# Kernel tuning notes

Hardware: AMD Instinct MI355X
Metric: run time of the kernel (lower is better)

## Reference

```python
import jax, jax.numpy as jnp
import numpy as np

N_NODES = 100000
N_EDGES = 1600000
HIDDEN = 128
NUM_FEAT = 1
NUM_CLASSES = 10
NUM_GRAPHS = 512


def setup_inputs() -> dict:
    key = jax.random.key(0)
    ks = jax.random.split(key, 16)
    x = jax.random.normal(ks[0], (N_NODES, NUM_FEAT), dtype=jnp.float32)
    edge_index = jax.random.randint(ks[1], (2, N_EDGES), 0, N_NODES, dtype=jnp.int64)
    batch = jnp.sort(jax.random.randint(ks[2], (N_NODES,), 0, NUM_GRAPHS, dtype=jnp.int64))
    def glorot(k, shape):
        lim = float(np.sqrt(6.0 / (shape[0] + shape[1])))
        return jax.random.uniform(k, shape, jnp.float32, -lim, lim)
    params = {
        'W1': glorot(ks[3], (NUM_FEAT, HIDDEN)), 'b1': jnp.zeros((HIDDEN,), jnp.float32),
        'W2': glorot(ks[4], (HIDDEN, HIDDEN)), 'b2': jnp.zeros((HIDDEN,), jnp.float32),
        'W3': glorot(ks[5], (HIDDEN, HIDDEN)), 'b3': jnp.zeros((HIDDEN,), jnp.float32),
        'W4': glorot(ks[6], (HIDDEN, HIDDEN)), 'b4': jnp.zeros((HIDDEN,), jnp.float32),
        'W5': glorot(ks[7], (HIDDEN, HIDDEN)), 'b5': jnp.zeros((HIDDEN,), jnp.float32),
        'Wlin': glorot(ks[8], (HIDDEN, NUM_CLASSES)), 'blin': jnp.zeros((NUM_CLASSES,), jnp.float32),
    }
    return {'x': x, 'edge_index': edge_index, 'batch': batch, **params}


def _gcn_norm(edge_index, n_nodes):
    # PyG GCNConv: add self-loops, sym-normalize by deg^-1/2 on both ends.
    loops = jnp.arange(n_nodes, dtype=edge_index.dtype)
    src = jnp.concatenate([edge_index[0], loops])
    dst = jnp.concatenate([edge_index[1], loops])
    deg = jax.ops.segment_sum(jnp.ones_like(dst, jnp.float32), dst, num_segments=n_nodes)
    dis = jnp.where(deg > 0, jax.lax.rsqrt(jnp.maximum(deg, 1.0)), 0.0)
    norm = dis[src] * dis[dst]  # [E + N]
    return src, dst, norm


def _gcn_conv(h, W, b, src, dst, norm, n_nodes):
    h = h @ W  # transform first (PyG order)
    msg = h[src] * norm[:, None]  # gather + scale, [E+N, H]
    out = jax.ops.segment_sum(msg, dst, num_segments=n_nodes)  # scatter-add
    return out + b


def reference(x, edge_index, batch, W1, b1, W2, b2, W3, b3, W4, b4, W5, b5, Wlin, blin):
    n = x.shape[0]
    src, dst, norm = _gcn_norm(edge_index, n)
    h = _gcn_conv(x, W1, b1, src, dst, norm, n)
    h = _gcn_conv(h, W2, b2, src, dst, norm, n)
    h = _gcn_conv(h, W3, b3, src, dst, norm, n)
    h = _gcn_conv(h, W4, b4, src, dst, norm, n)
    h = _gcn_conv(h, W5, b5, src, dst, norm, n)
    # global mean pool over graphs
    sums = jax.ops.segment_sum(h, batch, num_segments=NUM_GRAPHS)
    cnts = jax.ops.segment_sum(jnp.ones((n,), jnp.float32), batch, num_segments=NUM_GRAPHS)
    pooled = sums / jnp.maximum(cnts, 1.0)[:, None]
    # dropout is identity at eval
    return pooled @ Wlin + blin
```

## Files before the change

### kernel.cpp

```cpp
#include <hip/hip_runtime.h>

#define NT 256
#define BN_SHIFT 8
#define NBUCKET_MAX 512
#define CAP 8192
#define EPB 4096

__global__ void __launch_bounds__(768)
prep_kernel(const float* __restrict__ W1, const float* __restrict__ b1,
            const float* __restrict__ W2, const float* __restrict__ b2,
            const float* __restrict__ W3, const float* __restrict__ b3,
            const float* __restrict__ W4, const float* __restrict__ b4,
            const float* __restrict__ W5, const float* __restrict__ b5,
            const float* __restrict__ Wlin, float* __restrict__ qout,
            int* __restrict__ gcur, int NB) {
  __shared__ float cur[6][128];
  __shared__ float red[6][10][8];
  const int tid = threadIdx.x;
  for (int i = tid; i < NB; i += 768) gcur[i] = 0;
  const int vi = tid >> 7;
  const int t = tid & 127;
  float init;
  if (vi == 0) init = W1[t];
  else if (vi == 1) init = b1[t];
  else if (vi == 2) init = b2[t];
  else if (vi == 3) init = b3[t];
  else if (vi == 4) init = b4[t];
  else init = b5[t];
  cur[vi][t] = init;
  __syncthreads();
  const float* Ws[4] = {W2, W3, W4, W5};
  #pragma unroll
  for (int l = 0; l < 4; ++l) {
    const int nact = l + 2;
    float s = 0.f;
    if (vi < nact) {
      const float* __restrict__ W = Ws[l];
      #pragma unroll 64
      for (int k = 0; k < 128; ++k) s += cur[vi][k] * W[k * 128 + t];
    }
    __syncthreads();
    if (vi < nact) cur[vi][t] = s;
    __syncthreads();
  }
  if (tid < 480) {
    int v = tid / 80, rem = tid % 80, c = rem >> 3, pp = rem & 7;
    float s = 0.f;
    #pragma unroll
    for (int k = 0; k < 16; ++k) {
      int kk = pp * 16 + k;
      s += cur[v][kk] * Wlin[kk * 10 + c];
    }
    red[v][c][pp] = s;
  }
  __syncthreads();
  if (tid < 60) {
    int v = tid / 10, c = tid % 10;
    float s = 0.f;
    #pragma unroll
    for (int p = 0; p < 8; ++p) s += red[v][c][p];
    qout[v * 10 + c] = s;
  }
}

__global__ void binA_kernel(const int* __restrict__ ei, int* __restrict__ gcur,
                            unsigned int* __restrict__ dump, int E, int NB) {
  __shared__ unsigned int cnt[NBUCKET_MAX];
  __shared__ unsigned int base[NBUCKET_MAX];
  const int t = threadIdx.x;
  const int e0 = blockIdx.x * EPB;
  const bool vec_ok = ((E & 3) == 0);
  for (int b = t; b < NB; b += 256) cnt[b] = 0;
  __syncthreads();
  unsigned int slot[16];
  unsigned int dreg[16];
  #pragma unroll
  for (int jj = 0; jj < 4; ++jj) {
    int e = e0 + jj * 1024 + t * 4;
    if (vec_ok && e + 3 < E) {
      int4 d4 = *reinterpret_cast<const int4*>(&ei[E + e]);
      dreg[jj * 4 + 0] = (unsigned)d4.x;
      dreg[jj * 4 + 1] = (unsigned)d4.y;
      dreg[jj * 4 + 2] = (unsigned)d4.z;
      dreg[jj * 4 + 3] = (unsigned)d4.w;
      #pragma unroll
      for (int k = 0; k < 4; ++k)
        slot[jj * 4 + k] = atomicAdd(&cnt[dreg[jj * 4 + k] >> BN_SHIFT], 1u);
    } else {
      #pragma unroll
      for (int k = 0; k < 4; ++k) {
        int ee = e + k;
        if (ee < E) {
          unsigned d = (unsigned)ei[E + ee];
          dreg[jj * 4 + k] = d;
          slot[jj * 4 + k] = atomicAdd(&cnt[d >> BN_SHIFT], 1u);
        }
      }
    }
  }
  __syncthreads();
  for (int b = t; b < NB; b += 256) {
    unsigned int c = cnt[b];
    base[b] = c ? (unsigned int)atomicAdd(&gcur[b], (int)c) : 0u;
  }
  __syncthreads();
  #pragma unroll
  for (int jj = 0; jj < 4; ++jj) {
    int e = e0 + jj * 1024 + t * 4;
    unsigned s4v[4];
    bool fast = (vec_ok && e + 3 < E);
    if (fast) {
      int4 s4 = *reinterpret_cast<const int4*>(&ei[e]);
      s4v[0] = (unsigned)s4.x; s4v[1] = (unsigned)s4.y;
      s4v[2] = (unsigned)s4.z; s4v[3] = (unsigned)s4.w;
    }
    #pragma unroll
    for (int k = 0; k < 4; ++k) {
      int ee = e + k;
      if (ee < E) {
        unsigned s = fast ? s4v[k] : (unsigned)ei[ee];
        unsigned d = dreg[jj * 4 + k];
        unsigned b = d >> BN_SHIFT;
        unsigned pos = base[b] + slot[jj * 4 + k];
        if (pos < CAP)
          dump[(size_t)b * CAP + pos] = (s << BN_SHIFT) | (d & 255u);
      }
    }
  }
}

__global__ void binB_kernel(const unsigned int* __restrict__ dump,
                            const int* __restrict__ gcur,
                            const float* __restrict__ x, int* __restrict__ col,
                            int2* __restrict__ rl, float* __restrict__ dis2,
                            float* __restrict__ sq, float2* __restrict__ ta, int N) {
  __shared__ int cnt[256];
  __shared__ int sc[256];
  __shared__ int cur[256];
  const int b = blockIdx.x, t = threadIdx.x;
  cnt[t] = 0;
  __syncthreads();
  int total = gcur[b];
  if (total > CAP) total = CAP;
  const unsigned int* seg = dump + (size_t)b * CAP;
  unsigned wreg[CAP / 256];
  #pragma unroll
  for (int k = 0; k < CAP / 256; ++k) {
    int i = (k << 8) + t;
    if (i < total) {
      unsigned w = seg[i];
      wreg[k] = w;
      atomicAdd(&cnt[w & 255u], 1);
    }
  }
  __syncthreads();
  int v = cnt[t];
  sc[t] = v;
  __syncthreads();
  for (int off = 1; off < 256; off <<= 1) {
    int u = (t >= off) ? sc[t - off] : 0;
    __syncthreads();
    sc[t] += u;
    __syncthreads();
  }
  int rbase = b * CAP + sc[t] - v;
  cur[t] = rbase;
  __syncthreads();
  #pragma unroll
  for (int k = 0; k < CAP / 256; ++k) {
    int i = (k << 8) + t;
    if (i < total) {
      unsigned w = wreg[k];
      int slot = atomicAdd(&cur[w & 255u], 1);
      col[slot] = (int)(w >> BN_SHIFT);
    }
  }
  int node = (b << BN_SHIFT) + t;
  if (node < N) {
    rl[node] = make_int2(rbase, v);
    float dis = rsqrtf((float)v + 1.0f);
    dis2[node] = dis * dis;
    sq[node] = 1.0f / dis;
    ta[node] = make_float2(dis * x[node], dis);
  }
}

__global__ void gather_kernel(const int* __restrict__ col, const int2* __restrict__ rl,
                              const float* __restrict__ dis2,
                              const float2* __restrict__ tin, float2* __restrict__ tout,
                              float* __restrict__ ssave, int N) {
  int tid = blockIdx.x * blockDim.x + threadIdx.x;
  int node = tid >> 3, l8 = tid & 7;
  if (node >= N) return;
  int2 r = rl[node];
  float sx = 0.f, sy = 0.f;
  int j = l8;
  for (; j + 8 < r.y; j += 16) {
    int c0 = col[r.x + j];
    int c1 = col[r.x + j + 8];
    float2 a0 = tin[c0];
    float2 a1 = tin[c1];
    sx += a0.x + a1.x;
    sy += a0.y + a1.y;
  }
  if (j < r.y) {
    float2 a = tin[col[r.x + j]];
    sx += a.x;
    sy += a.y;
  }
  sx += __shfl_xor(sx, 1);
  sx += __shfl_xor(sx, 2);
  sx += __shfl_xor(sx, 4);
  sy += __shfl_xor(sy, 1);
  sy += __shfl_xor(sy, 2);
  sy += __shfl_xor(sy, 4);
  if (l8 == 0) {
    float2 ts = tin[node];
    float m = dis2[node];
    float oy = m * (sy + ts.y);
    tout[node] = make_float2(m * (sx + ts.x), oy);
    if (ssave) ssave[node] = oy;
  }
}

__device__ __forceinline__ int lower_bound_i(const int* a, int n, int key) {
  int lo = 0, hi = n;
  while (lo < hi) {
    int mid = (lo + hi) >> 1;
    if (a[mid] < key) lo = mid + 1; else hi = mid;
  }
  return lo;
}

__global__ void pool_kernel(const int* __restrict__ batch, int N,
                            const float2* __restrict__ t5, const float* __restrict__ s4,
                            const float* __restrict__ s3, const float* __restrict__ s2,
                            const float* __restrict__ s1, const float* __restrict__ sq,
                            const float* __restrict__ q, const float* __restrict__ blin,
                            float* __restrict__ out) {
  int g = blockIdx.x;
  __shared__ int sh[2];
  if (threadIdx.x == 0) {
    sh[0] = lower_bound_i(batch, N, g);
    sh[1] = lower_bound_i(batch, N, g + 1);
  }
  __syncthreads();
  int lo = sh[0], hi = sh[1];
  float a[5] = {0.f, 0.f, 0.f, 0.f, 0.f};
  for (int i = lo + threadIdx.x; i < hi; i += blockDim.x) {
    float qq = sq[i];
    a[0] += t5[i].x * qq;
    a[1] += s4[i] * qq;
    a[2] += s3[i] * qq;
    a[3] += s2[i] * qq;
    a[4] += s1[i] * qq;
  }
  __shared__ float red[4][5];
  __shared__ float m5[5];
  int lane = threadIdx.x & 63, wave = threadIdx.x >> 6;
  #pragma unroll
  for (int j = 0; j < 5; ++j)
    #pragma unroll
    for (int o = 32; o > 0; o >>= 1) a[j] += __shfl_down(a[j], o);
  if (lane == 0)
    #pragma unroll
    for (int j = 0; j < 5; ++j) red[wave][j] = a[j];
  __syncthreads();
  if (threadIdx.x == 0) {
    float denom = fmaxf((float)(hi - lo), 1.0f);
    #pragma unroll
    for (int j = 0; j < 5; ++j)
      m5[j] = (red[0][j] + red[1][j] + red[2][j] + red[3][j]) / denom;
  }
  __syncthreads();
  int t = threadIdx.x;
  if (t < 10) {
    out[g * 10 + t] = m5[0] * q[t] + m5[1] * q[10 + t] + m5[2] * q[20 + t] +
                      m5[3] * q[30 + t] + m5[4] * q[40 + t] + q[50 + t] + blin[t];
  }
}

extern "C" void kernel_launch(void* const* d_in, const int* in_sizes, int n_in,
                              void* d_out, int out_size, void* d_ws, size_t ws_size,
                              hipStream_t stream) {
  const float* x    = (const float*)d_in[0];
  const int*   ei   = (const int*)d_in[1];
  const int*   batch= (const int*)d_in[2];
  const float* W1   = (const float*)d_in[3];
  const float* b1   = (const float*)d_in[4];
  const float* W2   = (const float*)d_in[5];
  const float* b2   = (const float*)d_in[6];
  const float* W3   = (const float*)d_in[7];
  const float* b3   = (const float*)d_in[8];
  const float* W4   = (const float*)d_in[9];
  const float* b4   = (const float*)d_in[10];
  const float* W5   = (const float*)d_in[11];
  const float* b5   = (const float*)d_in[12];
  const float* Wlin = (const float*)d_in[13];
  const float* blin = (const float*)d_in[14];

  const int N  = in_sizes[0];
  const int E  = in_sizes[1] / 2;
  const int G  = out_size / 10;
  const int NB = (N + 255) >> BN_SHIFT;

  float* ws = (float*)d_ws;
  size_t off = 0;
  float2* ta   = (float2*)(ws + off); off += 2 * (size_t)N;
  float2* tb   = (float2*)(ws + off); off += 2 * (size_t)N;
  float*  dis2 = ws + off;            off += N;
  float*  sq   = ws + off;            off += N;
  float*  s1   = ws + off;            off += N;
  float*  s2   = ws + off;            off += N;
  float*  s3   = ws + off;            off += N;
  float*  s4   = ws + off;            off += N;
  float*  qv   = ws + off;            off += 64;
  if (off & 1) off++;
  int2* rl     = (int2*)(ws + off);   off += 2 * (size_t)N;
  int* gcur    = (int*)(ws + off);    off += NB;
  if (off & 1) off++;
  unsigned int* dump = (unsigned int*)(ws + off); off += (size_t)NB * CAP;
  int* col     = (int*)(ws + off);    off += (size_t)NB * CAP;
  (void)ws_size;

  const int gridA = (E + EPB - 1) / EPB;
  const int gridG = (8 * N + NT - 1) / NT;

  prep_kernel<<<1, 768, 0, stream>>>(W1, b1, W2, b2, W3, b3, W4, b4, W5, b5,
                                     Wlin, qv, gcur, NB);
  binA_kernel<<<gridA, 256, 0, stream>>>(ei, gcur, dump, E, NB);
  binB_kernel<<<NB, 256, 0, stream>>>(dump, gcur, x, col, rl, dis2, sq, ta, N);

  gather_kernel<<<gridG, NT, 0, stream>>>(col, rl, dis2, ta, tb, s1, N);
  gather_kernel<<<gridG, NT, 0, stream>>>(col, rl, dis2, tb, ta, s2, N);
  gather_kernel<<<gridG, NT, 0, stream>>>(col, rl, dis2, ta, tb, s3, N);
  gather_kernel<<<gridG, NT, 0, stream>>>(col, rl, dis2, tb, ta, s4, N);
  gather_kernel<<<gridG, NT, 0, stream>>>(col, rl, dis2, ta, tb, nullptr, N);

  pool_kernel<<<G, 256, 0, stream>>>(batch, N, tb, s4, s3, s2, s1, sq, qv, blin,
                                     (float*)d_out);
}
```

Before: 116.1 us.

## Replace CSR gather with per-bucket shared-memory atomic scatter over binned edges

binB no longer builds a CSR (col/rl) via counting sort and only computes degrees. The five propagation layers now read the bucketed edge dump directly: each 1024-thread block owns a 256-node bucket and accumulates neighbor values into shared memory with float atomics. The last layer skips the unused y channel. This removes the per-edge col write and the sort pass, but brings LDS atomic contention and non-deterministic float summation order.

After: 165.5 us. +42.5%, slower.

```diff
diff --git a/kernel.cpp b/kernel.cpp
--- a/kernel.cpp
+++ b/kernel.cpp
@@ -131,95 +131,76 @@
 
 __global__ void binB_kernel(const unsigned int* __restrict__ dump,
                             const int* __restrict__ gcur,
-                            const float* __restrict__ x, int* __restrict__ col,
-                            int2* __restrict__ rl, float* __restrict__ dis2,
+                            const float* __restrict__ x, float* __restrict__ dis2,
                             float* __restrict__ sq, float2* __restrict__ ta, int N) {
   __shared__ int cnt[256];
-  __shared__ int sc[256];
-  __shared__ int cur[256];
   const int b = blockIdx.x, t = threadIdx.x;
   cnt[t] = 0;
   __syncthreads();
   int total = gcur[b];
   if (total > CAP) total = CAP;
   const unsigned int* seg = dump + (size_t)b * CAP;
-  unsigned wreg[CAP / 256];
-  #pragma unroll
-  for (int k = 0; k < CAP / 256; ++k) {
-    int i = (k << 8) + t;
-    if (i < total) {
-      unsigned w = seg[i];
-      wreg[k] = w;
-      atomicAdd(&cnt[w & 255u], 1);
-    }
-  }
-  __syncthreads();
-  int v = cnt[t];
-  sc[t] = v;
-  __syncthreads();
-  for (int off = 1; off < 256; off <<= 1) {
-    int u = (t >= off) ? sc[t - off] : 0;
-    __syncthreads();
-    sc[t] += u;
-    __syncthreads();
-  }
-  int rbase = b * CAP + sc[t] - v;
-  cur[t] = rbase;
-  __syncthreads();
-  #pragma unroll
-  for (int k = 0; k < CAP / 256; ++k) {
-    int i = (k << 8) + t;
-    if (i < total) {
-      unsigned w = wreg[k];
-      int slot = atomicAdd(&cur[w & 255u], 1);
-      col[slot] = (int)(w >> BN_SHIFT);
-    }
-  }
+  for (int i = t; i < total; i += 256) atomicAdd(&cnt[seg[i] & 255u], 1);
+  __syncthreads();
   int node = (b << BN_SHIFT) + t;
   if (node < N) {
-    rl[node] = make_int2(rbase, v);
-    float dis = rsqrtf((float)v + 1.0f);
+    float dis = rsqrtf((float)cnt[t] + 1.0f);
     dis2[node] = dis * dis;
     sq[node] = 1.0f / dis;
     ta[node] = make_float2(dis * x[node], dis);
   }
 }
 
-__global__ void gather_kernel(const int* __restrict__ col, const int2* __restrict__ rl,
-                              const float* __restrict__ dis2,
-                              const float2* __restrict__ tin, float2* __restrict__ tout,
-                              float* __restrict__ ssave, int N) {
-  int tid = blockIdx.x * blockDim.x + threadIdx.x;
-  int node = tid >> 3, l8 = tid & 7;
-  if (node >= N) return;
-  int2 r = rl[node];
-  float sx = 0.f, sy = 0.f;
-  int j = l8;
-  for (; j + 8 < r.y; j += 16) {
-    int c0 = col[r.x + j];
-    int c1 = col[r.x + j + 8];
-    float2 a0 = tin[c0];
-    float2 a1 = tin[c1];
-    sx += a0.x + a1.x;
-    sy += a0.y + a1.y;
-  }
-  if (j < r.y) {
-    float2 a = tin[col[r.x + j]];
-    sx += a.x;
-    sy += a.y;
-  }
-  sx += __shfl_xor(sx, 1);
-  sx += __shfl_xor(sx, 2);
-  sx += __shfl_xor(sx, 4);
-  sy += __shfl_xor(sy, 1);
-  sy += __shfl_xor(sy, 2);
-  sy += __shfl_xor(sy, 4);
-  if (l8 == 0) {
-    float2 ts = tin[node];
-    float m = dis2[node];
-    float oy = m * (sy + ts.y);
-    tout[node] = make_float2(m * (sx + ts.x), oy);
-    if (ssave) ssave[node] = oy;
+template <bool LAST>
+__global__ void __launch_bounds__(1024)
+scatter_kernel(const unsigned int* __restrict__ dump, const int* __restrict__ gcur,
+               const float* __restrict__ dis2, const float2* __restrict__ tin,
+               float2* __restrict__ tout, float* __restrict__ ssave, int N) {
+  __shared__ float accx[256];
+  __shared__ float accy[256];
+  const int b = blockIdx.x, t = threadIdx.x;
+  if (t < 256) { accx[t] = 0.f; accy[t] = 0.f; }
+  __syncthreads();
+  int cnt = gcur[b];
+  if (cnt > CAP) cnt = CAP;
+  const unsigned int* seg = dump + (size_t)b * CAP;
+  for (int i0 = t * 4; i0 < cnt; i0 += 4096) {
+    if (i0 + 3 < cnt) {
+      uint4 w = *reinterpret_cast<const uint4*>(seg + i0);
+      float2 f0 = tin[w.x >> BN_SHIFT];
+      float2 f1 = tin[w.y >> BN_SHIFT];
+      float2 f2 = tin[w.z >> BN_SHIFT];
+      float2 f3 = tin[w.w >> BN_SHIFT];
+      atomicAdd(&accx[w.x & 255u], f0.x);
+      atomicAdd(&accx[w.y & 255u], f1.x);
+      atomicAdd(&accx[w.z & 255u], f2.x);
+      atomicAdd(&accx[w.w & 255u], f3.x);
+      if (!LAST) {
+        atomicAdd(&accy[w.x & 255u], f0.y);
+        atomicAdd(&accy[w.y & 255u], f1.y);
+        atomicAdd(&accy[w.z & 255u], f2.y);
+        atomicAdd(&accy[w.w & 255u], f3.y);
+      }
+    } else {
+      for (int i = i0; i < cnt; ++i) {
+        unsigned w = seg[i];
+        float2 f = tin[w >> BN_SHIFT];
+        atomicAdd(&accx[w & 255u], f.x);
+        if (!LAST) atomicAdd(&accy[w & 255u], f.y);
+      }
+    }
+  }
+  __syncthreads();
+  if (t < 256) {
+    int node = (b << BN_SHIFT) + t;
+    if (node < N) {
+      float2 ts = tin[node];
+      float m = dis2[node];
+      float ox = m * (accx[t] + ts.x);
+      float oy = LAST ? 0.f : m * (accy[t] + ts.y);
+      tout[node] = make_float2(ox, oy);
+      if (!LAST) ssave[node] = oy;
+    }
   }
 }
 
@@ -315,27 +296,23 @@
   float*  s3   = ws + off;            off += N;
   float*  s4   = ws + off;            off += N;
   float*  qv   = ws + off;            off += 64;
-  if (off & 1) off++;
-  int2* rl     = (int2*)(ws + off);   off += 2 * (size_t)N;
   int* gcur    = (int*)(ws + off);    off += NB;
-  if (off & 1) off++;
+  off = (off + 3) & ~(size_t)3;
   unsigned int* dump = (unsigned int*)(ws + off); off += (size_t)NB * CAP;
-  int* col     = (int*)(ws + off);    off += (size_t)NB * CAP;
   (void)ws_size;
 
   const int gridA = (E + EPB - 1) / EPB;
-  const int gridG = (8 * N + NT - 1) / NT;
 
   prep_kernel<<<1, 768, 0, stream>>>(W1, b1, W2, b2, W3, b3, W4, b4, W5, b5,
                                      Wlin, qv, gcur, NB);
   binA_kernel<<<gridA, 256, 0, stream>>>(ei, gcur, dump, E, NB);
-  binB_kernel<<<NB, 256, 0, stream>>>(dump, gcur, x, col, rl, dis2, sq, ta, N);
-
-  gather_kernel<<<gridG, NT, 0, stream>>>(col, rl, dis2, ta, tb, s1, N);
-  gather_kernel<<<gridG, NT, 0, stream>>>(col, rl, dis2, tb, ta, s2, N);
-  gather_kernel<<<gridG, NT, 0, stream>>>(col, rl, dis2, ta, tb, s3, N);
-  gather_kernel<<<gridG, NT, 0, stream>>>(col, rl, dis2, tb, ta, s4, N);
-  gather_kernel<<<gridG, NT, 0, stream>>>(col, rl, dis2, ta, tb, nullptr, N);
+  binB_kernel<<<NB, 256, 0, stream>>>(dump, gcur, x, dis2, sq, ta, N);
+
+  scatter_kernel<false><<<NB, 1024, 0, stream>>>(dump, gcur, dis2, ta, tb, s1, N);
+  scatter_kernel<false><<<NB, 1024, 0, stream>>>(dump, gcur, dis2, tb, ta, s2, N);
+  scatter_kernel<false><<<NB, 1024, 0, stream>>>(dump, gcur, dis2, ta, tb, s3, N);
+  scatter_kernel<false><<<NB, 1024, 0, stream>>>(dump, gcur, dis2, tb, ta, s4, N);
+  scatter_kernel<true ><<<NB, 1024, 0, stream>>>(dump, gcur, dis2, ta, tb, nullptr, N);
 
   pool_kernel<<<G, 256, 0, stream>>>(batch, N, tb, s4, s3, s2, s1, sq, qv, blin,
                                      (float*)d_out);
```
